# Kernel tuning notes

Measured on AMD Instinct MI355X. Metric: run time of the kernel, lower is better.

The kernel has to match this reference:

```python
import jax, jax.numpy as jnp
import numpy as np

H, W = 32, 32          # input_resolution
N = H * W
DIM = 256
DG = 128               # dim_group
NG = DIM // DG         # num_groups = 2
NH = 8                 # num_heads
DH = DIM // NH         # dim_head = 32
NHG = NH // NG         # heads per group = 4
KS = 5                 # offset kernel size
FACTOR = 2.0           # offset_range_factor
EPS = 1e-5


def get_reference(h, w):
    ry = jnp.linspace(0.5, h - 0.5, h) / h * 2.0 - 1.0
    rx = jnp.linspace(0.5, w - 0.5, w) / w * 2.0 - 1.0
    gy, gx = jnp.meshgrid(ry, rx, indexing='ij')
    return jnp.stack((gy, gx), axis=-1)  # [h, w, 2] = (y, x) in [-1, 1]


def grid_sample(img, grid):
    # torch F.grid_sample: bilinear, align_corners=True, padding_mode='zeros'
    # img: [B, C, Hi, Wi]; grid: [B, ..., 2] with (x, y) in [-1, 1]
    B, C, Hi, Wi = img.shape
    gs = grid.shape[1:-1]
    x = (grid[..., 0] + 1.0) * 0.5 * (Wi - 1)
    y = (grid[..., 1] + 1.0) * 0.5 * (Hi - 1)
    x0 = jnp.floor(x)
    y0 = jnp.floor(y)
    imgf = img.reshape(B, C, Hi * Wi)
    out = jnp.zeros((B, C, int(np.prod(gs))), img.dtype)
    for dy in (0, 1):
        for dx in (0, 1):
            yi = y0 + dy
            xi = x0 + dx
            wgt = (1.0 - jnp.abs(x - xi)) * (1.0 - jnp.abs(y - yi))
            valid = (yi >= 0) & (yi < Hi) & (xi >= 0) & (xi < Wi)
            yc = jnp.clip(yi, 0, Hi - 1).astype(jnp.int32)
            xc = jnp.clip(xi, 0, Wi - 1).astype(jnp.int32)
            idx = (yc * Wi + xc).reshape(B, 1, -1)
            g = jnp.take_along_axis(imgf, jnp.broadcast_to(idx, (B, C, idx.shape[-1])), axis=2)
            out = out + g * (wgt * valid).reshape(B, 1, -1)
    return out.reshape(B, C, *gs)


def setup_inputs() -> dict:
    key = jax.random.key(0)
    ks = jax.random.split(key, 10)
    s = 0.02
    return {
        'x': jax.random.normal(ks[0], (8, N, DIM), jnp.float32),
        'Wq': jax.random.normal(ks[1], (DIM, DIM), jnp.float32) * s,
        'Wkv': jax.random.normal(ks[2], (DIM, 2 * DIM), jnp.float32) * s,
        'conv_w': jax.random.normal(ks[3], (DG, 1, KS, KS), jnp.float32) * s,   # depthwise OIHW
        'conv_b': jnp.zeros((DG,), jnp.float32),
        'ln_g': jnp.ones((DG,), jnp.float32),
        'ln_b': jnp.zeros((DG,), jnp.float32),
        'Woff': jax.random.normal(ks[4], (DG, 2), jnp.float32) * s,
        'rpe': jax.random.normal(ks[5], (NH, 2 * H - 1, 2 * W - 1), jnp.float32) * 0.01,
        'Wout': jax.random.normal(ks[6], (DIM, DIM), jnp.float32) * s,
        'bout': jnp.zeros((DIM,), jnp.float32),
    }


def reference(x, Wq, Wkv, conv_w, conv_b, ln_g, ln_b, Woff, rpe, Wout, bout):
    B = x.shape[0]
    scale = DH ** (-0.5)
    ref = get_reference(H, W)  # [H, W, 2] (y, x)

    q = x @ Wq  # [B, N, DIM]

    # rearrange 'b (h w) (ng dg) -> (b ng) dg h w'
    xg = q.reshape(B, H, W, NG, DG).transpose(0, 3, 4, 1, 2).reshape(B * NG, DG, H, W)

    # conv_offset: depthwise conv -> LN -> GELU -> Linear(dg, 2)
    off = jax.lax.conv_general_dilated(
        xg, conv_w, (1, 1), [(KS // 2, KS // 2)] * 2,
        dimension_numbers=('NCHW', 'OIHW', 'NCHW'), feature_group_count=DG)
    off = off + conv_b[None, :, None, None]
    off = off.transpose(0, 2, 3, 1)  # [Bng, H, W, DG]
    mu = off.mean(-1, keepdims=True)
    var = ((off - mu) ** 2).mean(-1, keepdims=True)
    off = (off - mu) * jax.lax.rsqrt(var + EPS) * ln_g + ln_b
    off = jax.nn.gelu(off, approximate=False)
    offset = off @ Woff  # [Bng, H, W, 2] (y, x)
    offset = jnp.tanh(offset) * jnp.array([1.0 / H, 1.0 / W], jnp.float32) * FACTOR

    pos = offset + ref  # [Bng, H, W, 2] (y, x)

    # deformable sampling of q-feature map
    x_sampled = grid_sample(xg, pos[..., ::-1])  # [Bng, DG, H, W]
    # '(b ng) dg h w -> b (h w) (ng dg)'
    x_sampled = x_sampled.reshape(B, NG, DG, H * W).transpose(0, 3, 1, 2).reshape(B, N, NG * DG)

    # relative-position-bias lookup via grid_sample
    rpe_bias = jnp.broadcast_to(rpe.reshape(1, NG, NHG, 2 * H - 1, 2 * W - 1),
                                (B, NG, NHG, 2 * H - 1, 2 * W - 1)).reshape(B * NG, NHG, 2 * H - 1, 2 * W - 1)
    q_grid = ref.reshape(1, N, 1, 2)
    posr = pos.reshape(B * NG, 1, N, 2)
    disp = (q_grid - posr) * 0.5  # [Bng, N, N, 2]
    attn_bias = grid_sample(rpe_bias, disp[..., ::-1])  # [Bng, NHG, N, N]
    attn_bias = attn_bias.reshape(B, NG * NHG, N, N)     # [B, NH, N, N]

    kv = x_sampled @ Wkv
    k, v = kv[..., :DIM], kv[..., DIM:]
    qh = q.reshape(B, N, NH, DH).transpose(0, 2, 1, 3) * scale
    kh = k.reshape(B, N, NH, DH).transpose(0, 2, 1, 3)
    vh = v.reshape(B, N, NH, DH).transpose(0, 2, 1, 3)

    sim = jnp.einsum('bhid,bhjd->bhij', qh, kh) + attn_bias
    attn = jax.nn.softmax(sim, axis=-1)
    out = jnp.einsum('bhij,bhjd->bhid', attn, vh)
    out = out.transpose(0, 2, 1, 3).reshape(B, N, NH * DH)
    return out @ Wout + bout
```

## Files before the change

kernel.cpp:

```cpp
#include <hip/hip_runtime.h>
#include <hip/hip_bf16.h>
#include <hip/hip_fp16.h>
#include <hip/hip_fp8.h>


#define EPS_ 1e-5f
#define ASCALE 0.17677669529663687f
#define LOG2E  1.4426950408889634f

typedef __attribute__((ext_vector_type(8))) short bf16x8;
typedef __attribute__((ext_vector_type(4))) float f32x4;

__device__ __forceinline__ short f2bf(float f) {
  union { float f; unsigned u; } v; v.f = f;
  unsigned r = (v.u + 0x7fffu + ((v.u >> 16) & 1u)) >> 16;
  return (short)r;
}
__device__ __forceinline__ unsigned pk2bf(float a, float b) {
  union { __hip_bfloat162 h; unsigned u; } v;
  v.h = __float22bfloat162_rn(make_float2(a, b));
  return v.u;
}
__device__ __forceinline__ float exp2_fast(float x) {
  return __builtin_amdgcn_exp2f(x);
}

__device__ __forceinline__ unsigned pack_fp8_quad(float v00, float v10,
                                                  float v01, float v11) {
#if __has_builtin(__builtin_amdgcn_cvt_pk_fp8_f32)
  int r = 0;
  r = __builtin_amdgcn_cvt_pk_fp8_f32(v00, v10, r, false);
  r = __builtin_amdgcn_cvt_pk_fp8_f32(v01, v11, r, true);
  return (unsigned)r;
#else
  __hip_fp8x2_e4m3 elo(make_float2(v00, v10));
  __hip_fp8x2_e4m3 ehi(make_float2(v01, v11));
  return (unsigned)(unsigned short)elo.__x |
         ((unsigned)(unsigned short)ehi.__x << 16);
#endif
}
__device__ __forceinline__ void unpack_fp8_quad(unsigned u, float& g00,
                                                float& g10, float& g01,
                                                float& g11) {
#if __has_builtin(__builtin_amdgcn_cvt_pk_f32_fp8)
  auto ga = __builtin_amdgcn_cvt_pk_f32_fp8((int)u, false);
  auto gb = __builtin_amdgcn_cvt_pk_f32_fp8((int)u, true);
  g00 = ga[0]; g10 = ga[1]; g01 = gb[0]; g11 = gb[1];
#else
  __hip_fp8x2_e4m3 plo, phi;
  plo.__x = (__hip_fp8x2_storage_t)(unsigned short)(u & 0xffffu);
  phi.__x = (__hip_fp8x2_storage_t)(unsigned short)(u >> 16);
  float2 fa = (float2)plo, fb = (float2)phi;
  g00 = fa.x; g10 = fa.y; g01 = fb.x; g11 = fb.y;
#endif
}

__global__ __launch_bounds__(256) void prep_all(
    const float* __restrict__ Wkv, const float* __restrict__ Wout,
    const float* __restrict__ Wq, const float* __restrict__ rpe,
    short* __restrict__ Wkvt, short* __restrict__ Woutt,
    short* __restrict__ Wqt, unsigned* __restrict__ rpeq)
{
  int bid = blockIdx.x, k = threadIdx.x;
  if (bid >= 1024) {
    int i = (bid - 1024) * 256 + k;
    int h = i >> 12, idx = i & 4095;
    int ty = idx >> 6, tx = idx & 63;
    const float* rp = rpe + h * 3969;
    float v00 = 0.f, v10 = 0.f, v01 = 0.f, v11 = 0.f;
    if (tx <= 62) {
      if (ty <= 62) v00 = rp[ty * 63 + tx] * LOG2E;
      if (ty <= 61) v10 = rp[(ty + 1) * 63 + tx] * LOG2E;
    }
    if (tx <= 61) {
      if (ty <= 62) v01 = rp[ty * 63 + tx + 1] * LOG2E;
      if (ty <= 61) v11 = rp[(ty + 1) * 63 + tx + 1] * LOG2E;
    }
    rpeq[i] = pack_fp8_quad(v00, v10, v01, v11);
    return;
  }
  if (bid < 512) Wkvt[bid * 256 + k] = f2bf(Wkv[k * 512 + bid]);
  else if (bid < 768) { int n = bid - 512; Woutt[n * 256 + k] = f2bf(Wout[k * 256 + n]); }
  else { int n = bid - 768; Wqt[n * 256 + k] = f2bf(Wq[k * 256 + n]); }
}

__global__ __launch_bounds__(256) void gemm_bf16(
    const short* __restrict__ Ab, const float* __restrict__ Af,
    const short* __restrict__ Bt,
    float* __restrict__ Cf, short* __restrict__ Cb,
    const float* __restrict__ bias, int N)
{
  __shared__ __align__(16) short As[64 * 40];
  __shared__ __align__(16) short Bs[64 * 40];
  const int t = threadIdx.x;
  const int n0 = blockIdx.x << 6, m0 = blockIdx.y << 6;
  const int wv = t >> 6, l16 = t & 15, quad = (t & 63) >> 4;
  const int row = t >> 2, koff = (t & 3) << 3;

  auto loadA = [&](int k0) -> bf16x8 {
    if (Af) {
      const float* src = &Af[(size_t)(m0 + row) * 256 + k0 + koff];
      float4 f0 = *(const float4*)src;
      float4 f1 = *(const float4*)(src + 4);
      union { unsigned u[4]; bf16x8 v; } c;
      c.u[0] = pk2bf(f0.x, f0.y); c.u[1] = pk2bf(f0.z, f0.w);
      c.u[2] = pk2bf(f1.x, f1.y); c.u[3] = pk2bf(f1.z, f1.w);
      return c.v;
    }
    return *(const bf16x8*)&Ab[(size_t)(m0 + row) * 256 + k0 + koff];
  };

  f32x4 acc[4] = {};
  bf16x8 av = loadA(0);
  bf16x8 bv = *(const bf16x8*)&Bt[(size_t)(n0 + row) * 256 + koff];
  for (int k0 = 0; k0 < 256; k0 += 32) {
    __syncthreads();
    *(bf16x8*)&As[row * 40 + koff] = av;
    *(bf16x8*)&Bs[row * 40 + koff] = bv;
    __syncthreads();
    if (k0 + 32 < 256) {
      av = loadA(k0 + 32);
      bv = *(const bf16x8*)&Bt[(size_t)(n0 + row) * 256 + k0 + 32 + koff];
    }
    bf16x8 a = *(const bf16x8*)&As[((wv << 4) + l16) * 40 + (quad << 3)];
#pragma unroll
    for (int jt = 0; jt < 4; jt++) {
      bf16x8 bb = *(const bf16x8*)&Bs[((jt << 4) + l16) * 40 + (quad << 3)];
      acc[jt] = __builtin_amdgcn_mfma_f32_16x16x32_bf16(a, bb, acc[jt], 0, 0, 0);
    }
  }
#pragma unroll
  for (int jt = 0; jt < 4; jt++) {
#pragma unroll
    for (int r = 0; r < 4; r++) {
      int mrow = m0 + (wv << 4) + (quad << 2) + r;
      int ncol = n0 + (jt << 4) + l16;
      float v = acc[jt][r];
      if (bias) v += bias[ncol];
      if (Cf) Cf[(size_t)mrow * N + ncol] = v;
      else    Cb[(size_t)mrow * N + ncol] = f2bf(v);
    }
  }
}

__global__ __launch_bounds__(256) void conv_pos_sample_kernel(
    const float* __restrict__ q, const float* __restrict__ conv_w,
    const float* __restrict__ conv_b, const float* __restrict__ ln_g,
    const float* __restrict__ ln_b, const float* __restrict__ Woff,
    float* __restrict__ pos, short* __restrict__ xsb)
{
  const int p = (blockIdx.x << 2) + (threadIdx.x >> 6);
  const int lane = threadIdx.x & 63;
  const int bg = p >> 10, pix = p & 1023;
  const int hh = pix >> 5, ww = pix & 31;
  const int b = bg >> 1, g = bg & 1;
  const int c0 = lane << 1;
  const float* qbase = q + ((size_t)(b << 10) << 8) + (g << 7) + c0;

  float wr0[25], wr1[25];
  {
    const float* w0 = conv_w + c0 * 25;
#pragma unroll
    for (int i = 0; i < 25; i++) { wr0[i] = w0[i]; wr1[i] = w0[i + 25]; }
  }

  float2 cb = *(const float2*)&conv_b[c0];
  float a0 = cb.x, a1 = cb.y;
#pragma unroll
  for (int dy = 0; dy < 5; dy++) {
    int y = hh + dy - 2;
    int yc = y < 0 ? 0 : (y > 31 ? 31 : y);
    float my = ((unsigned)y < 32u) ? 1.f : 0.f;
#pragma unroll
    for (int dx = 0; dx < 5; dx++) {
      int x = ww + dx - 2;
      int xc = x < 0 ? 0 : (x > 31 ? 31 : x);
      float m = ((unsigned)x < 32u) ? my : 0.f;
      float2 qv = *(const float2*)&qbase[(size_t)((yc << 5) + xc) << 8];
      a0 = fmaf(qv.x * m, wr0[dy * 5 + dx], a0);
      a1 = fmaf(qv.y * m, wr1[dy * 5 + dx], a1);
    }
  }
  float s1 = a0 + a1, s2 = a0 * a0 + a1 * a1;
#pragma unroll
  for (int o = 32; o; o >>= 1) { s1 += __shfl_xor(s1, o); s2 += __shfl_xor(s2, o); }
  float mu = s1 * (1.f / 128.f);
  float inv = rsqrtf(fmaf(-mu, mu, s2 * (1.f / 128.f)) + EPS_);
  float2 lg = *(const float2*)&ln_g[c0];
  float2 lb = *(const float2*)&ln_b[c0];
  float v0 = (a0 - mu) * inv * lg.x + lb.x;
  float v1 = (a1 - mu) * inv * lg.y + lb.y;
  float ge0 = 0.5f * v0 * (1.f + erff(v0 * 0.70710678118654752f));
  float ge1 = 0.5f * v1 * (1.f + erff(v1 * 0.70710678118654752f));
  float2 W0 = *(const float2*)&Woff[c0 * 2];
  float2 W1 = *(const float2*)&Woff[c0 * 2 + 2];
  float o0 = ge0 * W0.x + ge1 * W1.x;
  float o1 = ge0 * W0.y + ge1 * W1.y;
#pragma unroll
  for (int o = 32; o; o >>= 1) { o0 += __shfl_xor(o0, o); o1 += __shfl_xor(o1, o); }
  float py = tanhf(o0) * 0.0625f + ((hh + 0.5f) * 0.0625f - 1.f);
  float px = tanhf(o1) * 0.0625f + ((ww + 0.5f) * 0.0625f - 1.f);
  if (lane == 0)
    ((float2*)pos)[(bg << 10) + pix] = make_float2(py, px);

  float x = (px + 1.f) * 15.5f;
  float y = (py + 1.f) * 15.5f;
  float x0f = floorf(x), y0f = floorf(y);
  int ix0 = (int)x0f, iy0 = (int)y0f;
  float fx = x - x0f, fy = y - y0f;
  float ac0 = 0.f, ac1 = 0.f;
#pragma unroll
  for (int dy = 0; dy < 2; dy++) {
#pragma unroll
    for (int dx = 0; dx < 2; dx++) {
      int yi = iy0 + dy, xi = ix0 + dx;
      int yc = yi < 0 ? 0 : (yi > 31 ? 31 : yi);
      int xc = xi < 0 ? 0 : (xi > 31 ? 31 : xi);
      float valid = ((unsigned)yi < 32u && (unsigned)xi < 32u) ? 1.f : 0.f;
      float w = (dy ? fy : 1.f - fy) * (dx ? fx : 1.f - fx) * valid;
      float2 qv = *(const float2*)&qbase[(size_t)((yc << 5) + xc) << 8];
      ac0 = fmaf(w, qv.x, ac0);
      ac1 = fmaf(w, qv.y, ac1);
    }
  }
  *(unsigned*)&xsb[(size_t)((b << 10) + pix) * 256 + (g << 7) + c0] = pk2bf(ac0, ac1);
}

__global__ __launch_bounds__(256, 4) void attn_kernel(
    const float* __restrict__ q, const short* __restrict__ kvb,
    const float* __restrict__ pos, const unsigned* __restrict__ rpeq,
    short* __restrict__ ao)
{
  const int it = blockIdx.x, h = blockIdx.y, b = blockIdx.z;
  const int g = h >> 2, t = threadIdx.x;
  const int wv = t >> 6, l16 = t & 15, quad = (t & 63) >> 4;

  __shared__ __align__(16) short PL[64 * 72];
  __shared__ __align__(16) short Vt[32 * 68];
  __shared__ float2 posT[64];
  __shared__ __align__(16) unsigned rpe8[64 * 64];

  {
    const unsigned* src = rpeq + (h << 12);
    for (int i = t; i < 4096; i += 256) rpe8[i] = src[i];
  }

  const int row0 = (it << 6) + (wv << 4);
  bf16x8 aq;
  {
    const float* src = q + (size_t)((b << 10) + row0 + l16) * 256 + (h << 5) + (quad << 3);
    float4 f0 = *(const float4*)src;
    float4 f1 = *(const float4*)(src + 4);
    const float sc = ASCALE * LOG2E;
    union { unsigned u[4]; bf16x8 v; } c;
    c.u[0] = pk2bf(f0.x * sc, f0.y * sc); c.u[1] = pk2bf(f0.z * sc, f0.w * sc);
    c.u[2] = pk2bf(f1.x * sc, f1.y * sc); c.u[3] = pk2bf(f1.z * sc, f1.w * sc);
    aq = c.v;
  }

  const float ayc = 15.5f * (((row0 >> 5) + 0.5f) * 0.0625f - 1.f) + 31.f;
  float ax[4];
#pragma unroll
  for (int r = 0; r < 4; r++) {
    int ix = (row0 & 31) + (quad << 2) + r;
    ax[r] = 15.5f * ((ix + 0.5f) * 0.0625f - 1.f) + 31.f;
  }

  bf16x8 vones;
#pragma unroll
  for (int i = 0; i < 8; i++) vones[i] = (short)0x3F80;

  const int vj = t & 63, vc = t >> 6;
  const short* vsrc = kvb + (size_t)((b << 10) + vj) * 512 + 256 + (h << 5) + (vc << 3);
  const short* ksrc = kvb + (size_t)((b << 10) + l16) * 512 + (h << 5) + (quad << 3);
  const float2* psrc = (const float2*)pos + (((b << 1) + g) << 10) + t;

  f32x4 Oacc[2] = {};
  f32x4 lacc = {};

  bf16x8 vv_cur = *(const bf16x8*)vsrc;
  vsrc += 32768;
  float2 pp_cur = make_float2(0.f, 0.f);
  if (t < 64) pp_cur = *psrc;
  psrc += 64;

  for (int kt = 0; kt < 16; kt++) {
    __syncthreads();
#pragma unroll
    for (int k2 = 0; k2 < 8; k2++) Vt[((vc << 3) + k2) * 68 + vj] = vv_cur[k2];
    if (t < 64)
      posT[t] = make_float2(-15.5f * pp_cur.x, -15.5f * pp_cur.y);
    __syncthreads();

    bf16x8 vv_nxt = vv_cur;
    float2 pp_nxt = pp_cur;
    if (kt < 15) {
      vv_nxt = *(const bf16x8*)vsrc;
      if (t < 64) pp_nxt = *psrc;
    }
    vsrc += 32768; psrc += 64;

    f32x4 S[4];
#pragma unroll
    for (int jt = 0; jt < 4; jt++) {
      bf16x8 bk = *(const bf16x8*)(ksrc + (size_t)jt * 8192);
      f32x4 z = {};
      S[jt] = __builtin_amdgcn_mfma_f32_16x16x32_bf16(aq, bk, z, 0, 0, 0);
    }

    float fyv[4];
    int ybv[4];
    float wyv[4];
#pragma unroll
    for (int jt = 0; jt < 4; jt++) {
      float2 bv = posT[(jt << 4) + l16];
      float ys = ayc + bv.x;
      float y0f = floorf(ys);
      fyv[jt] = ys - y0f;
      ybv[jt] = (int)y0f << 6;
      wyv[jt] = bv.y;
    }

    unsigned pu[4][2];
#pragma unroll
    for (int jt = 0; jt < 4; jt++) {
      float fy = fyv[jt];
      int ybase = ybv[jt];
      float pv[4];
#pragma unroll
      for (int r = 0; r < 4; r++) {
        float sx = ax[r] + wyv[jt];
        float x0f = floorf(sx);
        float fx = sx - x0f;
        unsigned u = rpe8[ybase + (int)x0f];
        float g00, g10, g01, g11;
        unpack_fp8_quad(u, g00, g10, g01, g11);
        float h0 = fmaf(fx, g01 - g00, g00);
        float h1 = fmaf(fx, g11 - g10, g10);
        float bias = fmaf(fy, h1 - h0, h0);
        pv[r] = exp2_fast(S[jt][r] + bias);
      }
      pu[jt][0] = pk2bf(pv[0], pv[1]);
      pu[jt][1] = pk2bf(pv[2], pv[3]);
    }

#pragma unroll
    for (int jt = 0; jt < 4; jt++) {
      int cb = (jt << 4) + l16;
      int rb = ((wv << 4) + (quad << 2)) * 72 + cb;
      PL[rb]       = (short)(pu[jt][0] & 0xffff);
      PL[rb + 72]  = (short)(pu[jt][0] >> 16);
      PL[rb + 144] = (short)(pu[jt][1] & 0xffff);
      PL[rb + 216] = (short)(pu[jt][1] >> 16);
    }
    bf16x8 pa0 = *(const bf16x8*)&PL[((wv << 4) + l16) * 72 + (quad << 3)];
    bf16x8 pa1 = *(const bf16x8*)&PL[((wv << 4) + l16) * 72 + 32 + (quad << 3)];
#pragma unroll
    for (int dt = 0; dt < 2; dt++) {
      bf16x8 vb0 = *(const bf16x8*)&Vt[((dt << 4) + l16) * 68 + (quad << 3)];
      bf16x8 vb1 = *(const bf16x8*)&Vt[((dt << 4) + l16) * 68 + 32 + (quad << 3)];
      Oacc[dt] = __builtin_amdgcn_mfma_f32_16x16x32_bf16(pa0, vb0, Oacc[dt], 0, 0, 0);
      Oacc[dt] = __builtin_amdgcn_mfma_f32_16x16x32_bf16(pa1, vb1, Oacc[dt], 0, 0, 0);
    }
    lacc = __builtin_amdgcn_mfma_f32_16x16x32_bf16(pa0, vones, lacc, 0, 0, 0);
    lacc = __builtin_amdgcn_mfma_f32_16x16x32_bf16(pa1, vones, lacc, 0, 0, 0);

    if (kt < 15) {
      uint4 p4 = __builtin_bit_cast(uint4, vv_nxt);
      asm volatile("" :: "v"(p4.x), "v"(p4.y), "v"(p4.z), "v"(p4.w),
                         "v"(pp_nxt.x), "v"(pp_nxt.y));
    }
    vv_cur = vv_nxt;
    pp_cur = pp_nxt;
    ksrc += 32768;
  }

#pragma unroll
  for (int r = 0; r < 4; r++) {
    float inv = 1.f / lacc[r];
    int row = row0 + (quad << 2) + r;
#pragma unroll
    for (int dt = 0; dt < 2; dt++) {
      ao[(size_t)((b << 10) + row) * 256 + (h << 5) + (dt << 4) + l16] =
          f2bf(Oacc[dt][r] * inv);
    }
  }
}

extern "C" void kernel_launch(void* const* d_in, const int* in_sizes, int n_in,
                              void* d_out, int out_size, void* d_ws, size_t ws_size,
                              hipStream_t stream) {
  (void)in_sizes; (void)n_in; (void)out_size; (void)ws_size;
  const float* x      = (const float*)d_in[0];
  const float* Wq     = (const float*)d_in[1];
  const float* Wkv    = (const float*)d_in[2];
  const float* conv_w = (const float*)d_in[3];
  const float* conv_b = (const float*)d_in[4];
  const float* ln_g   = (const float*)d_in[5];
  const float* ln_b   = (const float*)d_in[6];
  const float* Woff   = (const float*)d_in[7];
  const float* rpe    = (const float*)d_in[8];
  const float* Wout   = (const float*)d_in[9];
  const float* bout   = (const float*)d_in[10];
  float* out = (float*)d_out;

  float* ws      = (float*)d_ws;
  float* q       = ws;
  float* pos     = ws + 2097152;
  short* kvb     = (short*)(ws + 2129920);
  short* xsb     = (short*)(ws + 4227072);
  short* aob     = (short*)(ws + 5275648);
  short* Wkvt    = (short*)(ws + 6324224);
  short* Woutt   = (short*)(ws + 6389760);
  short* Wqt     = (short*)(ws + 6422528);
  unsigned* rpeq = (unsigned*)(ws + 6455296);

  prep_all<<<1152, 256, 0, stream>>>(Wkv, Wout, Wq, rpe, Wkvt, Woutt, Wqt, rpeq);
  gemm_bf16<<<dim3(4, 128), 256, 0, stream>>>(nullptr, x, Wqt, q, nullptr, nullptr, 256);
  conv_pos_sample_kernel<<<4096, 256, 0, stream>>>(q, conv_w, conv_b, ln_g, ln_b,
                                                   Woff, pos, xsb);
  gemm_bf16<<<dim3(8, 128), 256, 0, stream>>>(xsb, nullptr, Wkvt, nullptr, kvb, nullptr, 512);
  attn_kernel<<<dim3(16, 8, 8), 256, 0, stream>>>(q, kvb, pos, rpeq, aob);
  gemm_bf16<<<dim3(4, 128), 256, 0, stream>>>(aob, nullptr, Woutt, out, nullptr, bout, 256);
}
```

Baseline: 187.2 us.

## Write V transposed from KV GEMM epilogue and drop LDS staging in attention

The KV projection GEMM now writes the V half in a transposed [b, dim, token] bf16 layout through an LDS transpose in its epilogue. The attention kernel then reads V operands and positions directly from global memory, which removes the per-tile LDS staging, the register prefetch and both barriers per key tile. The cost is extra global and L2 reads with no software prefetch, plus an additional workspace buffer.

After: 206.6 us. 1.1x slower.

```diff
diff --git a/kernel.cpp b/kernel.cpp
--- a/kernel.cpp
+++ b/kernel.cpp
@@ -88,10 +88,11 @@
     const short* __restrict__ Ab, const float* __restrict__ Af,
     const short* __restrict__ Bt,
     float* __restrict__ Cf, short* __restrict__ Cb,
-    const float* __restrict__ bias, int N)
+    const float* __restrict__ bias, int N, short* __restrict__ vt)
 {
-  __shared__ __align__(16) short As[64 * 40];
-  __shared__ __align__(16) short Bs[64 * 40];
+  __shared__ __align__(16) short smem[5120];
+  short* As = smem;
+  short* Bs = smem + 2560;
   const int t = threadIdx.x;
   const int n0 = blockIdx.x << 6, m0 = blockIdx.y << 6;
   const int wv = t >> 6, l16 = t & 15, quad = (t & 63) >> 4;
@@ -129,6 +130,30 @@
       acc[jt] = __builtin_amdgcn_mfma_f32_16x16x32_bf16(a, bb, acc[jt], 0, 0, 0);
     }
   }
+
+  if (vt && n0 >= 256) {
+    __syncthreads();
+    short* sV = smem;
+#pragma unroll
+    for (int jt = 0; jt < 4; jt++) {
+#pragma unroll
+      for (int r = 0; r < 4; r++) {
+        int nl = (jt << 4) + l16;
+        int ml = (wv << 4) + (quad << 2) + r;
+        sV[nl * 72 + ml] = f2bf(acc[jt][r]);
+      }
+    }
+    __syncthreads();
+    int dl = t >> 2, js0 = (t & 3) << 3;
+    bf16x8 v0 = *(const bf16x8*)&sV[dl * 72 + js0];
+    bf16x8 v1 = *(const bf16x8*)&sV[dl * 72 + js0 + 32];
+    int bb = m0 >> 10, j0 = m0 & 1023;
+    size_t base = ((size_t)((bb << 8) + (n0 - 256) + dl) << 10) + j0;
+    *(bf16x8*)&vt[base + js0]      = v0;
+    *(bf16x8*)&vt[base + js0 + 32] = v1;
+    return;
+  }
+
 #pragma unroll
   for (int jt = 0; jt < 4; jt++) {
 #pragma unroll
@@ -228,16 +253,14 @@
 
 __global__ __launch_bounds__(256, 4) void attn_kernel(
     const float* __restrict__ q, const short* __restrict__ kvb,
-    const float* __restrict__ pos, const unsigned* __restrict__ rpeq,
-    short* __restrict__ ao)
+    const short* __restrict__ vtb, const float* __restrict__ pos,
+    const unsigned* __restrict__ rpeq, short* __restrict__ ao)
 {
   const int it = blockIdx.x, h = blockIdx.y, b = blockIdx.z;
   const int g = h >> 2, t = threadIdx.x;
   const int wv = t >> 6, l16 = t & 15, quad = (t & 63) >> 4;
 
   __shared__ __align__(16) short PL[64 * 72];
-  __shared__ __align__(16) short Vt[32 * 68];
-  __shared__ float2 posT[64];
   __shared__ __align__(16) unsigned rpe8[64 * 64];
 
   {
@@ -270,36 +293,16 @@
 #pragma unroll
   for (int i = 0; i < 8; i++) vones[i] = (short)0x3F80;
 
-  const int vj = t & 63, vc = t >> 6;
-  const short* vsrc = kvb + (size_t)((b << 10) + vj) * 512 + 256 + (h << 5) + (vc << 3);
   const short* ksrc = kvb + (size_t)((b << 10) + l16) * 512 + (h << 5) + (quad << 3);
-  const float2* psrc = (const float2*)pos + (((b << 1) + g) << 10) + t;
+  const short* vsrc = vtb + (((size_t)((b << 8) + (h << 5) + l16)) << 10) + (quad << 3);
+  const float2* psrc = (const float2*)pos + (((b << 1) + g) << 10) + l16;
 
   f32x4 Oacc[2] = {};
   f32x4 lacc = {};
 
-  bf16x8 vv_cur = *(const bf16x8*)vsrc;
-  vsrc += 32768;
-  float2 pp_cur = make_float2(0.f, 0.f);
-  if (t < 64) pp_cur = *psrc;
-  psrc += 64;
+  __syncthreads();
 
   for (int kt = 0; kt < 16; kt++) {
-    __syncthreads();
-#pragma unroll
-    for (int k2 = 0; k2 < 8; k2++) Vt[((vc << 3) + k2) * 68 + vj] = vv_cur[k2];
-    if (t < 64)
-      posT[t] = make_float2(-15.5f * pp_cur.x, -15.5f * pp_cur.y);
-    __syncthreads();
-
-    bf16x8 vv_nxt = vv_cur;
-    float2 pp_nxt = pp_cur;
-    if (kt < 15) {
-      vv_nxt = *(const bf16x8*)vsrc;
-      if (t < 64) pp_nxt = *psrc;
-    }
-    vsrc += 32768; psrc += 64;
-
     f32x4 S[4];
 #pragma unroll
     for (int jt = 0; jt < 4; jt++) {
@@ -308,28 +311,19 @@
       S[jt] = __builtin_amdgcn_mfma_f32_16x16x32_bf16(aq, bk, z, 0, 0, 0);
     }
 
-    float fyv[4];
-    int ybv[4];
-    float wyv[4];
+    unsigned pu[4][2];
 #pragma unroll
     for (int jt = 0; jt < 4; jt++) {
-      float2 bv = posT[(jt << 4) + l16];
-      float ys = ayc + bv.x;
+      float2 pp = psrc[jt << 4];
+      float ys = fmaf(-15.5f, pp.x, ayc);
       float y0f = floorf(ys);
-      fyv[jt] = ys - y0f;
-      ybv[jt] = (int)y0f << 6;
-      wyv[jt] = bv.y;
-    }
-
-    unsigned pu[4][2];
-#pragma unroll
-    for (int jt = 0; jt < 4; jt++) {
-      float fy = fyv[jt];
-      int ybase = ybv[jt];
+      float fy = ys - y0f;
+      int ybase = (int)y0f << 6;
+      float wy = -15.5f * pp.y;
       float pv[4];
 #pragma unroll
       for (int r = 0; r < 4; r++) {
-        float sx = ax[r] + wyv[jt];
+        float sx = ax[r] + wy;
         float x0f = floorf(sx);
         float fx = sx - x0f;
         unsigned u = rpe8[ybase + (int)x0f];
@@ -355,24 +349,21 @@
     }
     bf16x8 pa0 = *(const bf16x8*)&PL[((wv << 4) + l16) * 72 + (quad << 3)];
     bf16x8 pa1 = *(const bf16x8*)&PL[((wv << 4) + l16) * 72 + 32 + (quad << 3)];
+
 #pragma unroll
     for (int dt = 0; dt < 2; dt++) {
-      bf16x8 vb0 = *(const bf16x8*)&Vt[((dt << 4) + l16) * 68 + (quad << 3)];
-      bf16x8 vb1 = *(const bf16x8*)&Vt[((dt << 4) + l16) * 68 + 32 + (quad << 3)];
+      const short* vb = vsrc + ((size_t)dt << 14);
+      bf16x8 vb0 = *(const bf16x8*)vb;
+      bf16x8 vb1 = *(const bf16x8*)(vb + 32);
       Oacc[dt] = __builtin_amdgcn_mfma_f32_16x16x32_bf16(pa0, vb0, Oacc[dt], 0, 0, 0);
       Oacc[dt] = __builtin_amdgcn_mfma_f32_16x16x32_bf16(pa1, vb1, Oacc[dt], 0, 0, 0);
     }
     lacc = __builtin_amdgcn_mfma_f32_16x16x32_bf16(pa0, vones, lacc, 0, 0, 0);
     lacc = __builtin_amdgcn_mfma_f32_16x16x32_bf16(pa1, vones, lacc, 0, 0, 0);
 
-    if (kt < 15) {
-      uint4 p4 = __builtin_bit_cast(uint4, vv_nxt);
-      asm volatile("" :: "v"(p4.x), "v"(p4.y), "v"(p4.z), "v"(p4.w),
-                         "v"(pp_nxt.x), "v"(pp_nxt.y));
-    }
-    vv_cur = vv_nxt;
-    pp_cur = pp_nxt;
     ksrc += 32768;
+    vsrc += 64;
+    psrc += 64;
   }
 
 #pragma unroll
@@ -414,12 +405,13 @@
   short* Woutt   = (short*)(ws + 6389760);
   short* Wqt     = (short*)(ws + 6422528);
   unsigned* rpeq = (unsigned*)(ws + 6455296);
+  short* vtb     = (short*)(ws + 6488064);
 
   prep_all<<<1152, 256, 0, stream>>>(Wkv, Wout, Wq, rpe, Wkvt, Woutt, Wqt, rpeq);
-  gemm_bf16<<<dim3(4, 128), 256, 0, stream>>>(nullptr, x, Wqt, q, nullptr, nullptr, 256);
+  gemm_bf16<<<dim3(4, 128), 256, 0, stream>>>(nullptr, x, Wqt, q, nullptr, nullptr, 256, nullptr);
   conv_pos_sample_kernel<<<4096, 256, 0, stream>>>(q, conv_w, conv_b, ln_g, ln_b,
                                                    Woff, pos, xsb);
-  gemm_bf16<<<dim3(8, 128), 256, 0, stream>>>(xsb, nullptr, Wkvt, nullptr, kvb, nullptr, 512);
-  attn_kernel<<<dim3(16, 8, 8), 256, 0, stream>>>(q, kvb, pos, rpeq, aob);
-  gemm_bf16<<<dim3(4, 128), 256, 0, stream>>>(aob, nullptr, Woutt, out, nullptr, bout, 256);
-}
+  gemm_bf16<<<dim3(8, 128), 256, 0, stream>>>(xsb, nullptr, Wkvt, nullptr, kvb, nullptr, 512, vtb);
+  attn_kernel<<<dim3(16, 8, 8), 256, 0, stream>>>(q, kvb, vtb, pos, rpeq, aob);
+  gemm_bf16<<<dim3(4, 128), 256, 0, stream>>>(aob, nullptr, Woutt, out, nullptr, bout, 256, nullptr);
+}
```
